# Performance work log

Hardware: AMD Instinct MI355X
Metric: run time of the kernel (lower is better)

## Reference

```python
import jax, jax.numpy as jnp
import numpy as np

B_CAPS, C_CAPS, P_VEC, L_VEC, WIN, ITERS = 1024, 16, 16, 64, 4, 2
BATCH = 4
LOG_2PI = float(np.log(2.0 * np.pi))


def setup_inputs() -> dict:
    key = jax.random.key(0)
    k1, k2, k3, k4 = jax.random.split(key, 4)
    # x packs pose (16*B channels) and activation (B channels)
    x = jax.random.normal(k1, (BATCH, (P_VEC + 1) * B_CAPS, WIN, WIN), dtype=jnp.float32)
    W = 0.01 * jax.random.normal(k2, (C_CAPS, B_CAPS, L_VEC, P_VEC), dtype=jnp.float32)
    beta_v = jax.random.normal(k3, (1,), dtype=jnp.float32)
    beta_a = jax.random.normal(k4, (C_CAPS,), dtype=jnp.float32)
    return {"x": x, "W": W, "beta_v": beta_v, "beta_a": beta_a, "lambda_": jnp.float32(1.0)}


def reference(x, W, beta_v, beta_a, lambda_):
    b = x.shape[0]
    B, C, P, L, K = B_CAPS, C_CAPS, P_VEC, L_VEC, WIN
    N = B * K * K  # total input capsules (every spatial position of every prim capsule)
    # pose: (b, B, K, K, P); activation: (b, N)
    pose = x[:, : P * B].reshape(b, P, B, K, K).transpose(0, 2, 3, 4, 1)
    act = x[:, P * B :].reshape(b, N)
    # votes[b,i,x,y,c,l] = sum_p W[c,i,l,p] * pose[b,i,x,y,p]
    votes = jnp.einsum("cilp,bixyp->bixycl", W, pose)
    V = votes.reshape(b, N, C, L)
    a = act[:, :, None]  # (b, N, 1)
    R = jnp.full((b, N, C), 1.0 / C, dtype=x.dtype)
    mu = a_c = None
    for _ in range(ITERS):
        # ---- M-step: weighted mean / variance over input capsules ----
        r_hat = jnp.clip(R * a, 0.01)                 # (b,N,C)
        sum_r = r_hat.sum(axis=1)                     # (b,C)
        mu = jnp.einsum("bnc,bncl->bcl", r_hat, V) / sum_r[:, :, None]
        sigma = jnp.einsum("bnc,bncl->bcl", r_hat, (V - mu[:, None]) ** 2) / sum_r[:, :, None]
        sigma = jnp.clip(sigma, 0.01)
        cost = (beta_v + jnp.log(sigma)) * sum_r[:, :, None]          # (b,C,L)
        a_c = jax.nn.sigmoid(lambda_ * (beta_a[None, :] - cost.sum(-1)))  # (b,C)
        # ---- E-step (detached in the original: R round-trips through numpy) ----
        # p = prod_l exp(-(V-mu)^2)/sqrt(2*pi*sigma); R = a_c*p / sum_c a_c*p
        # computed in log-space (same math, numerically stable softmax form)
        logp = (-(V - mu[:, None]) ** 2 - 0.5 * (LOG_2PI + jnp.log(sigma[:, None]))).sum(-1)
        R = jax.lax.stop_gradient(jax.nn.softmax(jnp.log(a_c)[:, None, :] + logp, axis=-1))
    mus = mu.reshape(b, C * L, 1, 1)
    acts = a_c.reshape(b, C, 1, 1)
    return jnp.concatenate([mus, acts], axis=1)  # (b, C*L + C, 1, 1)
```

## Files before the change

### kernel.cpp

```cpp
#include <hip/hip_runtime.h>

#define LOG_2PI_F 1.8378770664093453f

constexpr int BC = 1024, CC = 16, PV = 16, LV = 64, BB = 4;
constexpr int CH = (PV + 1) * BC;
constexpr int SLAB = BB * CC * LV;
constexpr int SLABTOT = 2 * SLAB + BB * CC;
constexpr int NB2 = 512;
constexpr int NSLAB_SM = 32;
constexpr size_t WBF_ELEMS = (size_t)CC * BC * LV * PV;
constexpr size_t POSE_ELEMS = (size_t)BC * 64 * 16;
constexpr size_t ACT_ELEMS = (size_t)BC * 64;

typedef __attribute__((ext_vector_type(4))) short short4v;
typedef __attribute__((ext_vector_type(8))) short short8v;
typedef __attribute__((ext_vector_type(16))) float f32x16;

union ABfrag { short8v v; short4v h[2]; unsigned short u[8]; };

__device__ __forceinline__ unsigned short f2bf(float f) {
  unsigned u = __float_as_uint(f);
  u += 0x7fffu + ((u >> 16) & 1u);
  return (unsigned short)(u >> 16);
}

__device__ __forceinline__ short8v cvt8(const float4 a, const float4 b) {
  ABfrag f;
  f.u[0] = f2bf(a.x); f.u[1] = f2bf(a.y); f.u[2] = f2bf(a.z); f.u[3] = f2bf(a.w);
  f.u[4] = f2bf(b.x); f.u[5] = f2bf(b.y); f.u[6] = f2bf(b.z); f.u[7] = f2bf(b.w);
  return f.v;
}

template <int PASS>
__global__ __launch_bounds__(512, 4) void em_sweep2(
    const float* __restrict__ x, const float* __restrict__ W,
    const float* __restrict__ SredIn, const float* __restrict__ beta_v,
    const float* __restrict__ beta_a, const float* __restrict__ lam,
    float* __restrict__ Spart,
    unsigned short* __restrict__ WbfC, unsigned short* __restrict__ poseC,
    float* __restrict__ actC) {
  const int bid = blockIdx.x, t = threadIdx.x;
  const int w = t >> 6, lane = t & 63;
  const int ln31 = lane & 31, h = lane >> 5;
  const int cbase = 2 * w;

  float* slab = Spart + (size_t)bid * SLABTOT;

  __shared__ __align__(16) unsigned short pbf[2][64][20];
  __shared__ float act_s[2][64];
  __shared__ float T_s[64];
  __shared__ float sr_s[64];
  __shared__ float sc_s[64][17];
  __shared__ float rh2[16][64];
  __shared__ __align__(16) float mu_s[64][64];
  __shared__ float lsum_s[64][8];
  __shared__ float Sacc[SLABTOT];

  if (PASS == 1) {
    if (t < 256) {
      const int cap = t >> 7, tt = t & 127;
      const int r = tt >> 1, half = tt & 1;
      const int i = bid + cap * NB2;
      const int4 v = *reinterpret_cast<const int4*>(
          poseC + ((size_t)i * 64 + r) * 16 + 8 * half);
      union { int4 q; short4v s[2]; } u;
      u.q = v;
      *reinterpret_cast<short4v*>(&pbf[cap][r][8 * half]) = u.s[0];
      *reinterpret_cast<short4v*>(&pbf[cap][r][8 * half + 4]) = u.s[1];
    }
    if (t < 128) {
      const int cap = t >> 6, r = t & 63;
      act_s[cap][r] = actC[(size_t)(bid + cap * NB2) * 64 + r];
    }
    if (t < 64) sr_s[t] = 0.f;
    {
      const int bc = t >> 3, part = t & 7;
      const float inv = 1.f / SredIn[2 * SLAB + bc];
      float lsl = 0.f;
#pragma unroll
      for (int q = 0; q < 8; ++q) {
        const int idx = bc * 64 + part * 8 + q;
        const float m = SredIn[idx] * inv;
        const float s2 = fmaxf(SredIn[SLAB + idx] * inv - m * m, 0.01f);
        lsl += logf(s2);
        mu_s[bc][part * 8 + q] = m;
      }
      lsum_s[bc][part] = lsl;
    }
    __syncthreads();
    if (t < 64) {
      float lsum = 0.f;
#pragma unroll
      for (int q = 0; q < 8; ++q) lsum += lsum_s[t][q];
      const float sr = SredIn[2 * SLAB + t];
      const float z = lam[0] * (beta_a[t & 15] - (64.f * beta_v[0] + lsum) * sr);
      const float ac = 1.f / (1.f + expf(-z));
      T_s[t] = logf(ac) - 0.5f * (64.f * LOG_2PI_F + lsum);
    }
    __syncthreads();
  } else {
    {
      const int cap = t >> 8, tt = t & 255;
      const int b = tt >> 6, p = (tt >> 2) & 15, q = tt & 3;
      const int i = bid + cap * NB2;
      const float4 v = *reinterpret_cast<const float4*>(
          x + ((size_t)(b * CH + p * BC + i)) * 16 + 4 * q);
      pbf[cap][b * 16 + 4 * q + 0][p] = f2bf(v.x);
      pbf[cap][b * 16 + 4 * q + 1][p] = f2bf(v.y);
      pbf[cap][b * 16 + 4 * q + 2][p] = f2bf(v.z);
      pbf[cap][b * 16 + 4 * q + 3][p] = f2bf(v.w);
    }
    if (t < 128) {
      const int cap = t >> 6, r = t & 63;
      const int b = r >> 4, xy = r & 15;
      const float a = x[((size_t)(b * CH + PV * BC + bid + cap * NB2)) * 16 + xy];
      act_s[cap][r] = a;
      actC[(size_t)(bid + cap * NB2) * 64 + r] = a;
    }
    __syncthreads();
    if (t < 256) {
      const int cap = t >> 7, tt = t & 127;
      const int r = tt >> 1, half = tt & 1;
      const int i = bid + cap * NB2;
      union { int4 q; short4v s[2]; } u;
      u.s[0] = *reinterpret_cast<const short4v*>(&pbf[cap][r][8 * half]);
      u.s[1] = *reinterpret_cast<const short4v*>(&pbf[cap][r][8 * half + 4]);
      *reinterpret_cast<int4*>(poseC + ((size_t)i * 64 + r) * 16 + 8 * half) = u.q;
    }
  }

  const f32x16 zero16 = {};

#pragma unroll
  for (int cap = 0; cap < 2; ++cap) {
    const int i = bid + cap * NB2;
    short8v wf[4];
    if (PASS == 1) {
#pragma unroll
      for (int k = 0; k < 4; ++k) {
        const int cl_ = k >> 1, lh = k & 1;
        const size_t off = ((size_t)(cbase + cl_) * BC + i) * 1024 +
                           (lh * 32 + ln31) * 16 + 8 * h;
        wf[k] = *reinterpret_cast<const short8v*>(WbfC + off);
      }
    } else {
#pragma unroll
      for (int k = 0; k < 4; ++k) {
        const int cl_ = k >> 1, lh = k & 1;
        const float* src = W + ((size_t)(cbase + cl_) * BC + i) * 1024 +
                           (lh * 32 + ln31) * 16 + 8 * h;
        const float4 v0 = *reinterpret_cast<const float4*>(src);
        const float4 v1 = *reinterpret_cast<const float4*>(src + 4);
        wf[k] = cvt8(v0, v1);
      }
    }
#pragma unroll
    for (int k = 0; k < 4; ++k) asm volatile("" : "+v"(wf[k]));
    if (PASS == 0) {
#pragma unroll
      for (int k = 0; k < 4; ++k) {
        const int cl_ = k >> 1, lh = k & 1;
        const size_t off = ((size_t)(cbase + cl_) * BC + i) * 1024 +
                           (lh * 32 + ln31) * 16 + 8 * h;
        *reinterpret_cast<short8v*>(WbfC + off) = wf[k];
      }
    }

    if (PASS == 1) {
#pragma unroll
      for (int rowhalf = 0; rowhalf < 2; ++rowhalf) {
        ABfrag A;
        {
          const int r = rowhalf * 32 + ln31;
          A.h[0] = *reinterpret_cast<const short4v*>(&pbf[cap][r][8 * h]);
          A.h[1] = *reinterpret_cast<const short4v*>(&pbf[cap][r][8 * h + 4]);
        }
        const int b = (rowhalf * 32 + ln31) >> 4;
#pragma unroll
        for (int cl_ = 0; cl_ < 2; ++cl_) {
          float sc = 0.f;
#pragma unroll
          for (int lh = 0; lh < 2; ++lh) {
            const f32x16 acc = __builtin_amdgcn_mfma_f32_32x32x16_bf16(
                wf[cl_ * 2 + lh], A.v, zero16, 0, 0, 0);
            const float* mrow = &mu_s[b * CC + cbase + cl_][lh * 32 + 4 * h];
#pragma unroll
            for (int g = 0; g < 4; ++g) {
              const float4 m4 = *reinterpret_cast<const float4*>(mrow + 8 * g);
              float d;
              d = acc[4 * g + 0] - m4.x; sc = fmaf(d, d, sc);
              d = acc[4 * g + 1] - m4.y; sc = fmaf(d, d, sc);
              d = acc[4 * g + 2] - m4.z; sc = fmaf(d, d, sc);
              d = acc[4 * g + 3] - m4.w; sc = fmaf(d, d, sc);
            }
          }
          sc += __shfl_xor(sc, 32, 64);
          if (h == 0) sc_s[rowhalf * 32 + ln31][cbase + cl_] = sc;
        }
      }
      __syncthreads();
      {
        const int r = t & 63, cq = t >> 6, b = r >> 4;
        float s[16];
#pragma unroll
        for (int cc = 0; cc < 16; ++cc) s[cc] = T_s[b * CC + cc] - sc_s[r][cc];
        float m = s[0];
#pragma unroll
        for (int cc = 1; cc < 16; ++cc) m = fmaxf(m, s[cc]);
        float den = 0.f;
#pragma unroll
        for (int cc = 0; cc < 16; ++cc) { s[cc] = __expf(s[cc] - m); den += s[cc]; }
        const float a = act_s[cap][r] / den;
#pragma unroll
        for (int k = 0; k < 2; ++k) {
          const int cc = 2 * cq + k;
          const float rh = fmaxf(s[cc] * a, 0.01f);
          rh2[cc][r] = rh;
          atomicAdd(&sr_s[b * CC + cc], rh);
        }
      }
      __syncthreads();
    }

#pragma unroll
    for (int pair = 0; pair < 2; ++pair) {
      ABfrag A;
      {
        const int r = pair * 32 + ln31;
        A.h[0] = *reinterpret_cast<const short4v*>(&pbf[cap][r][8 * h]);
        A.h[1] = *reinterpret_cast<const short4v*>(&pbf[cap][r][8 * h + 4]);
      }
      float p1[4][2] = {}, p2[4][2] = {};
#pragma unroll
      for (int cl_ = 0; cl_ < 2; ++cl_) {
        float rq[16];
        if (PASS == 1) {
#pragma unroll
          for (int g = 0; g < 4; ++g) {
            const float4 v = *reinterpret_cast<const float4*>(
                &rh2[cbase + cl_][pair * 32 + 8 * g + 4 * h]);
            rq[4 * g + 0] = v.x; rq[4 * g + 1] = v.y;
            rq[4 * g + 2] = v.z; rq[4 * g + 3] = v.w;
          }
        } else {
#pragma unroll
          for (int g = 0; g < 4; ++g) {
            const float4 v = *reinterpret_cast<const float4*>(
                &act_s[cap][pair * 32 + 8 * g + 4 * h]);
            rq[4 * g + 0] = fmaxf(v.x * 0.0625f, 0.01f);
            rq[4 * g + 1] = fmaxf(v.y * 0.0625f, 0.01f);
            rq[4 * g + 2] = fmaxf(v.z * 0.0625f, 0.01f);
            rq[4 * g + 3] = fmaxf(v.w * 0.0625f, 0.01f);
          }
        }
#pragma unroll
        for (int lh = 0; lh < 2; ++lh) {
          const f32x16 acc = __builtin_amdgcn_mfma_f32_32x32x16_bf16(
              A.v, wf[cl_ * 2 + lh], zero16, 0, 0, 0);
          const int t4 = cl_ * 2 + lh;
#pragma unroll
          for (int j = 0; j < 16; ++j) {
            const float v = acc[j];
            const float rv = rq[j] * v;
            p1[t4][j >> 3] += rv;
            p2[t4][j >> 3] = fmaf(rv, v, p2[t4][j >> 3]);
          }
        }
      }
#pragma unroll
      for (int t4 = 0; t4 < 4; ++t4)
#pragma unroll
        for (int bh = 0; bh < 2; ++bh) {
          float v1 = p1[t4][bh]; v1 += __shfl_xor(v1, 32, 64);
          float v2 = p2[t4][bh]; v2 += __shfl_xor(v2, 32, 64);
          const int b = pair * 2 + bh, c = cbase + (t4 >> 1);
          const int idx = (b * CC + c) * LV + (t4 & 1) * 32 + ln31;
          if (h == 0) {
            if (cap == 0) { Sacc[idx] = v1; Sacc[SLAB + idx] = v2; }
            else          { Sacc[idx] += v1; Sacc[SLAB + idx] += v2; }
          }
        }
    }
  }

  if (PASS == 1) {
    if (t < 64) Sacc[2 * SLAB + t] = sr_s[t];
  } else {
    if (t < 64) {
      const int b = t >> 4;
      float s = 0.f;
#pragma unroll
      for (int cp = 0; cp < 2; ++cp)
#pragma unroll
        for (int xy = 0; xy < 16; ++xy)
          s += fmaxf(act_s[cp][b * 16 + xy] * 0.0625f, 0.01f);
      Sacc[2 * SLAB + t] = s;
    }
  }
  __syncthreads();
  for (int idx = t; idx < SLABTOT; idx += 512) slab[idx] = Sacc[idx];
}

__global__ void reduce_stageA(const float* __restrict__ Spart,
                              float* __restrict__ Spart2) {
  const int idx = blockIdx.x * 256 + threadIdx.x;
  if (idx >= SLABTOT) return;
  const float* base = Spart + (size_t)(blockIdx.y * 32) * SLABTOT + idx;
  float a = 0.f;
#pragma unroll 8
  for (int s = 0; s < 32; ++s) a += base[(size_t)s * SLABTOT];
  Spart2[(size_t)blockIdx.y * SLABTOT + idx] = a;
}

__global__ void reduce_stageB(const float* __restrict__ Spart2,
                              float* __restrict__ Sred, int nchunk) {
  const int idx = blockIdx.x * 256 + threadIdx.x;
  if (idx >= SLABTOT) return;
  float a = 0.f;
  for (int s = 0; s < nchunk; ++s) a += Spart2[(size_t)s * SLABTOT + idx];
  Sred[idx] = a;
}

__global__ void stats_final(const float* __restrict__ Sred,
                            const float* __restrict__ beta_v,
                            const float* __restrict__ beta_a,
                            const float* __restrict__ lam,
                            float* __restrict__ out) {
  __shared__ float lsum_s[64][8];
  const int t = threadIdx.x;
  const int bc = t >> 3, part = t & 7;
  const float inv = 1.f / Sred[2 * SLAB + bc];
  float lsl = 0.f;
#pragma unroll
  for (int q = 0; q < 8; ++q) {
    const int l = part * 8 + q;
    const int idx = bc * 64 + l;
    const float m = Sred[idx] * inv;
    const float s2 = fmaxf(Sred[SLAB + idx] * inv - m * m, 0.01f);
    lsl += logf(s2);
    out[(size_t)(bc >> 4) * 1040 + (bc & 15) * 64 + l] = m;
  }
  lsum_s[bc][part] = lsl;
  __syncthreads();
  if (t < 64) {
    float lsum = 0.f;
#pragma unroll
    for (int q = 0; q < 8; ++q) lsum += lsum_s[t][q];
    const float sr = Sred[2 * SLAB + t];
    const float z = lam[0] * (beta_a[t & 15] - (64.f * beta_v[0] + lsum) * sr);
    out[(size_t)(t >> 4) * 1040 + 1024 + (t & 15)] = 1.f / (1.f + expf(-z));
  }
}

template <int PASS>
__global__ __launch_bounds__(512, 4) void em_sweep_legacy(
    const float* __restrict__ x, const float* __restrict__ W,
    const float* __restrict__ mu, const float* __restrict__ T,
    float* __restrict__ Spart, int nslab) {
  const int i = blockIdx.x, t = threadIdx.x;
  const int w = t >> 6, lane = t & 63;
  const int ln31 = lane & 31, h = lane >> 5;
  const int cbase = 2 * w;

  float* S1p = Spart + (size_t)(i % nslab) * SLABTOT;
  float* S2p = S1p + SLAB;
  float* Srp = S1p + 2 * SLAB;

  __shared__ __align__(16) unsigned short pbf[64][20];
  __shared__ float act_s[64];
  __shared__ float T_s[64];
  __shared__ float sr_s[64];
  __shared__ float sc_s[64][17];
  __shared__ float rh2[16][64];
  __shared__ __align__(16) float mu_s[64][64];

  short8v wf[4];
#pragma unroll
  for (int k = 0; k < 4; ++k) {
    const int cl_ = k >> 1, lh = k & 1;
    const float* src = W + ((size_t)(cbase + cl_) * BC + i) * 1024 +
                       (lh * 32 + ln31) * 16 + 8 * h;
    const float4 v0 = *reinterpret_cast<const float4*>(src);
    const float4 v1 = *reinterpret_cast<const float4*>(src + 4);
    wf[k] = cvt8(v0, v1);
  }
#pragma unroll
  for (int k = 0; k < 4; ++k) asm volatile("" : "+v"(wf[k]));

  if (t < 256) {
    const int b = t >> 6, p = (t >> 2) & 15, q = t & 3;
    const float4 v = *reinterpret_cast<const float4*>(
        x + ((size_t)(b * CH + p * BC + i)) * 16 + 4 * q);
    pbf[b * 16 + 4 * q + 0][p] = f2bf(v.x);
    pbf[b * 16 + 4 * q + 1][p] = f2bf(v.y);
    pbf[b * 16 + 4 * q + 2][p] = f2bf(v.z);
    pbf[b * 16 + 4 * q + 3][p] = f2bf(v.w);
  }
  if (t < 64) {
    const int b = t >> 4, xy = t & 15;
    act_s[t] = x[((size_t)(b * CH + PV * BC + i)) * 16 + xy];
    if (PASS == 1) { T_s[t] = T[t]; sr_s[t] = 0.f; }
  }
  if (PASS == 1) {
    const float4* msrc = reinterpret_cast<const float4*>(mu);
    float4* mdst = reinterpret_cast<float4*>(&mu_s[0][0]);
    mdst[t] = msrc[t];
    mdst[t + 512] = msrc[t + 512];
  }
  __syncthreads();

  const f32x16 zero16 = {};

  if (PASS == 1) {
#pragma unroll
    for (int rowhalf = 0; rowhalf < 2; ++rowhalf) {
      ABfrag A;
      {
        const int r = rowhalf * 32 + ln31;
        A.h[0] = *reinterpret_cast<const short4v*>(&pbf[r][8 * h]);
        A.h[1] = *reinterpret_cast<const short4v*>(&pbf[r][8 * h + 4]);
      }
      const int b = (rowhalf * 32 + ln31) >> 4;
#pragma unroll
      for (int cl_ = 0; cl_ < 2; ++cl_) {
        float sc = 0.f;
#pragma unroll
        for (int lh = 0; lh < 2; ++lh) {
          const f32x16 acc = __builtin_amdgcn_mfma_f32_32x32x16_bf16(
              wf[cl_ * 2 + lh], A.v, zero16, 0, 0, 0);
          const float* mrow = &mu_s[b * CC + cbase + cl_][lh * 32 + 4 * h];
#pragma unroll
          for (int g = 0; g < 4; ++g) {
            const float4 m4 = *reinterpret_cast<const float4*>(mrow + 8 * g);
            float d;
            d = acc[4 * g + 0] - m4.x; sc = fmaf(d, d, sc);
            d = acc[4 * g + 1] - m4.y; sc = fmaf(d, d, sc);
            d = acc[4 * g + 2] - m4.z; sc = fmaf(d, d, sc);
            d = acc[4 * g + 3] - m4.w; sc = fmaf(d, d, sc);
          }
        }
        sc += __shfl_xor(sc, 32, 64);
        if (h == 0) sc_s[rowhalf * 32 + ln31][cbase + cl_] = sc;
      }
    }
    __syncthreads();
    {
      const int r = t & 63, cq = t >> 6, b = r >> 4;
      float s[16];
#pragma unroll
      for (int cc = 0; cc < 16; ++cc) s[cc] = T_s[b * CC + cc] - sc_s[r][cc];
      float m = s[0];
#pragma unroll
      for (int cc = 1; cc < 16; ++cc) m = fmaxf(m, s[cc]);
      float den = 0.f;
#pragma unroll
      for (int cc = 0; cc < 16; ++cc) { s[cc] = __expf(s[cc] - m); den += s[cc]; }
      const float a = act_s[r] / den;
#pragma unroll
      for (int k = 0; k < 2; ++k) {
        const int cc = 2 * cq + k;
        const float rh = fmaxf(s[cc] * a, 0.01f);
        rh2[cc][r] = rh;
        atomicAdd(&sr_s[b * CC + cc], rh);
      }
    }
    __syncthreads();
  }

#pragma unroll
  for (int pair = 0; pair < 2; ++pair) {
    ABfrag A;
    {
      const int r = pair * 32 + ln31;
      A.h[0] = *reinterpret_cast<const short4v*>(&pbf[r][8 * h]);
      A.h[1] = *reinterpret_cast<const short4v*>(&pbf[r][8 * h + 4]);
    }
    float p1[4][2] = {}, p2[4][2] = {};
#pragma unroll
    for (int cl_ = 0; cl_ < 2; ++cl_) {
      float rq[16];
      if (PASS == 1) {
#pragma unroll
        for (int g = 0; g < 4; ++g) {
          const float4 v = *reinterpret_cast<const float4*>(
              &rh2[cbase + cl_][pair * 32 + 8 * g + 4 * h]);
          rq[4 * g + 0] = v.x; rq[4 * g + 1] = v.y;
          rq[4 * g + 2] = v.z; rq[4 * g + 3] = v.w;
        }
      } else {
#pragma unroll
        for (int g = 0; g < 4; ++g) {
          const float4 v = *reinterpret_cast<const float4*>(
              &act_s[pair * 32 + 8 * g + 4 * h]);
          rq[4 * g + 0] = fmaxf(v.x * 0.0625f, 0.01f);
          rq[4 * g + 1] = fmaxf(v.y * 0.0625f, 0.01f);
          rq[4 * g + 2] = fmaxf(v.z * 0.0625f, 0.01f);
          rq[4 * g + 3] = fmaxf(v.w * 0.0625f, 0.01f);
        }
      }
#pragma unroll
      for (int lh = 0; lh < 2; ++lh) {
        const f32x16 acc = __builtin_amdgcn_mfma_f32_32x32x16_bf16(
            A.v, wf[cl_ * 2 + lh], zero16, 0, 0, 0);
        const int t4 = cl_ * 2 + lh;
#pragma unroll
        for (int j = 0; j < 16; ++j) {
          const float v = acc[j];
          const float rv = rq[j] * v;
          p1[t4][j >> 3] += rv;
          p2[t4][j >> 3] = fmaf(rv, v, p2[t4][j >> 3]);
        }
      }
    }
#pragma unroll
    for (int t4 = 0; t4 < 4; ++t4)
#pragma unroll
      for (int bh = 0; bh < 2; ++bh) {
        float v1 = p1[t4][bh]; v1 += __shfl_xor(v1, 32, 64);
        float v2 = p2[t4][bh]; v2 += __shfl_xor(v2, 32, 64);
        const int b = pair * 2 + bh, c = cbase + (t4 >> 1);
        const int idx = (b * CC + c) * LV + (t4 & 1) * 32 + ln31;
        if (h == 0) { atomicAdd(&S1p[idx], v1); atomicAdd(&S2p[idx], v2); }
      }
  }

  if (PASS == 1) {
    if (t < 64) atomicAdd(&Srp[t], sr_s[t]);
  } else {
    if (t < 64) {
      const int b = t >> 4;
      float s = 0.f;
#pragma unroll
      for (int xy = 0; xy < 16; ++xy) s += fmaxf(act_s[b * 16 + xy] * 0.0625f, 0.01f);
      atomicAdd(&Srp[t], s);
    }
  }
}

__global__ void reduce_slabs(const float* __restrict__ Spart, float* __restrict__ Sred,
                             int nslab, int chunk) {
  const int idx = blockIdx.x * 256 + threadIdx.x;
  if (idx >= SLABTOT) return;
  const int s0 = blockIdx.y * chunk;
  const int s1 = min(s0 + chunk, nslab);
  float a = 0.f;
#pragma unroll 8
  for (int s = s0; s < s1; s++) a += Spart[(size_t)s * SLABTOT + idx];
  atomicAdd(&Sred[idx], a);
}

template <int FINAL>
__global__ void stats_post(const float* __restrict__ Sred,
                           const float* __restrict__ beta_v,
                           const float* __restrict__ beta_a,
                           const float* __restrict__ lam,
                           float* __restrict__ mu_out, float* __restrict__ T_out,
                           float* __restrict__ out) {
  __shared__ float lsum_s[64][8];
  const int t = threadIdx.x;
  const int bc = t >> 3, part = t & 7;
  const float inv = 1.f / Sred[2 * SLAB + bc];
  float lsl = 0.f;
#pragma unroll
  for (int q = 0; q < 8; ++q) {
    const int l = part * 8 + q;
    const int idx = bc * 64 + l;
    const float m = Sred[idx] * inv;
    const float s2 = fmaxf(Sred[SLAB + idx] * inv - m * m, 0.01f);
    lsl += logf(s2);
    if (FINAL) out[(size_t)(bc >> 4) * 1040 + (bc & 15) * 64 + l] = m;
    else mu_out[idx] = m;
  }
  lsum_s[bc][part] = lsl;
  __syncthreads();
  if (t < 64) {
    float lsum = 0.f;
#pragma unroll
    for (int q = 0; q < 8; ++q) lsum += lsum_s[t][q];
    const float sr = Sred[2 * SLAB + t];
    const float z = lam[0] * (beta_a[t & 15] - (64.f * beta_v[0] + lsum) * sr);
    const float ac = 1.f / (1.f + expf(-z));
    if (FINAL) out[(size_t)(t >> 4) * 1040 + 1024 + (t & 15)] = ac;
    else T_out[t] = logf(ac) - 0.5f * (64.f * LOG_2PI_F + lsum);
  }
}

extern "C" void kernel_launch(void* const* d_in, const int* in_sizes, int n_in,
                              void* d_out, int out_size, void* d_ws, size_t ws_size,
                              hipStream_t stream) {
  const float* x = (const float*)d_in[0];
  const float* W = (const float*)d_in[1];
  const float* beta_v = (const float*)d_in[2];
  const float* beta_a = (const float*)d_in[3];
  const float* lam = (const float*)d_in[4];
  float* out = (float*)d_out;

  const size_t need_cache =
      ((size_t)NB2 * SLABTOT + SLABTOT) * sizeof(float) + WBF_ELEMS * 2 +
      POSE_ELEMS * 2 + ACT_ELEMS * sizeof(float) +
      (size_t)16 * SLABTOT * sizeof(float);

  float* Spart = (float*)d_ws;

  if (ws_size >= need_cache) {
    float* Sred = Spart + (size_t)NB2 * SLABTOT;
    unsigned short* WbfC = (unsigned short*)(Sred + SLABTOT);
    unsigned short* poseC = WbfC + WBF_ELEMS;
    float* actC = (float*)(poseC + POSE_ELEMS);
    float* Spart2 = actC + ACT_ELEMS;

    const dim3 agrid((SLABTOT + 255) / 256, 16);
    const dim3 bgrid((SLABTOT + 255) / 256);
    em_sweep2<0><<<dim3(NB2), dim3(512), 0, stream>>>(
        x, W, nullptr, beta_v, beta_a, lam, Spart, WbfC, poseC, actC);
    reduce_stageA<<<agrid, dim3(256), 0, stream>>>(Spart, Spart2);
    reduce_stageB<<<bgrid, dim3(256), 0, stream>>>(Spart2, Sred, 16);
    em_sweep2<1><<<dim3(NB2), dim3(512), 0, stream>>>(
        x, W, Sred, beta_v, beta_a, lam, Spart, WbfC, poseC, actC);
    reduce_stageA<<<agrid, dim3(256), 0, stream>>>(Spart, Spart2);
    reduce_stageB<<<bgrid, dim3(256), 0, stream>>>(Spart2, Sred, 16);
    stats_final<<<dim3(1), dim3(512), 0, stream>>>(Sred, beta_v, beta_a, lam, out);
    return;
  }

  const int nslab = NSLAB_SM;
  float* Sred = Spart + (size_t)nslab * SLABTOT;
  float* muW = Sred + SLABTOT;
  float* Tw = muW + SLAB;
  const int chunk = 32;
  const dim3 rgrid((SLABTOT + 255) / 256, (nslab + chunk - 1) / chunk);

  hipMemsetAsync(Spart, 0, (size_t)nslab * SLABTOT * sizeof(float), stream);
  hipMemsetAsync(Sred, 0, SLABTOT * sizeof(float), stream);
  em_sweep_legacy<0><<<dim3(BC), dim3(512), 0, stream>>>(x, W, nullptr, nullptr, Spart, nslab);
  reduce_slabs<<<rgrid, dim3(256), 0, stream>>>(Spart, Sred, nslab, chunk);
  stats_post<0><<<dim3(1), dim3(512), 0, stream>>>(Sred, beta_v, beta_a, lam, muW, Tw, nullptr);

  hipMemsetAsync(Spart, 0, (size_t)nslab * SLABTOT * sizeof(float), stream);
  em_sweep_legacy<1><<<dim3(BC), dim3(512), 0, stream>>>(x, W, muW, Tw, Spart, nslab);
  hipMemsetAsync(Sred, 0, SLABTOT * sizeof(float), stream);
  reduce_slabs<<<rgrid, dim3(256), 0, stream>>>(Spart, Sred, nslab, chunk);
  stats_post<1><<<dim3(1), dim3(512), 0, stream>>>(Sred, beta_v, beta_a, lam, nullptr, nullptr, out);
}
```

Baseline: 80.66 us.

## Use 1024-thread blocks with one output capsule per wave in EM sweep

The block size of both EM sweep launches doubles from 512 to 1024 threads, so each of 16 waves handles one output capsule instead of two. Per-wave work and register footprint for weight fragments and accumulators are halved, which is meant to expose more parallelism and latency hiding. The cost is more waves contending for the same LDS, more synchronisation per block, and possibly lower blocks per CU given the shared memory footprint. Setup phases that assume 512 threads are guarded with t<512.

```diff
diff --git a/kernel.cpp b/kernel.cpp
--- a/kernel.cpp
+++ b/kernel.cpp
@@ -32,7 +32,7 @@
 }
 
 template <int PASS>
-__global__ __launch_bounds__(512, 4) void em_sweep2(
+__global__ __launch_bounds__(1024, 4) void em_sweep2(
     const float* __restrict__ x, const float* __restrict__ W,
     const float* __restrict__ SredIn, const float* __restrict__ beta_v,
     const float* __restrict__ beta_a, const float* __restrict__ lam,
@@ -40,9 +40,10 @@
     unsigned short* __restrict__ WbfC, unsigned short* __restrict__ poseC,
     float* __restrict__ actC) {
   const int bid = blockIdx.x, t = threadIdx.x;
-  const int w = t >> 6, lane = t & 63;
+  const int w = t >> 6;
+  const int lane = t & 63;
   const int ln31 = lane & 31, h = lane >> 5;
-  const int cbase = 2 * w;
+  const int c = w;
 
   float* slab = Spart + (size_t)bid * SLABTOT;
 
@@ -73,7 +74,7 @@
       act_s[cap][r] = actC[(size_t)(bid + cap * NB2) * 64 + r];
     }
     if (t < 64) sr_s[t] = 0.f;
-    {
+    if (t < 512) {
       const int bc = t >> 3, part = t & 7;
       const float inv = 1.f / SredIn[2 * SLAB + bc];
       float lsl = 0.f;
@@ -99,7 +100,7 @@
     }
     __syncthreads();
   } else {
-    {
+    if (t < 512) {
       const int cap = t >> 8, tt = t & 255;
       const int b = tt >> 6, p = (tt >> 2) & 15, q = tt & 3;
       const int i = bid + cap * NB2;
@@ -134,34 +135,31 @@
 #pragma unroll
   for (int cap = 0; cap < 2; ++cap) {
     const int i = bid + cap * NB2;
-    short8v wf[4];
+    short8v wf[2];
     if (PASS == 1) {
 #pragma unroll
-      for (int k = 0; k < 4; ++k) {
-        const int cl_ = k >> 1, lh = k & 1;
-        const size_t off = ((size_t)(cbase + cl_) * BC + i) * 1024 +
-                           (lh * 32 + ln31) * 16 + 8 * h;
+      for (int k = 0; k < 2; ++k) {
+        const size_t off = ((size_t)c * BC + i) * 1024 +
+                           (k * 32 + ln31) * 16 + 8 * h;
         wf[k] = *reinterpret_cast<const short8v*>(WbfC + off);
       }
     } else {
 #pragma unroll
-      for (int k = 0; k < 4; ++k) {
-        const int cl_ = k >> 1, lh = k & 1;
-        const float* src = W + ((size_t)(cbase + cl_) * BC + i) * 1024 +
-                           (lh * 32 + ln31) * 16 + 8 * h;
+      for (int k = 0; k < 2; ++k) {
+        const float* src = W + ((size_t)c * BC + i) * 1024 +
+                           (k * 32 + ln31) * 16 + 8 * h;
         const float4 v0 = *reinterpret_cast<const float4*>(src);
         const float4 v1 = *reinterpret_cast<const float4*>(src + 4);
         wf[k] = cvt8(v0, v1);
       }
     }
 #pragma unroll
-    for (int k = 0; k < 4; ++k) asm volatile("" : "+v"(wf[k]));
+    for (int k = 0; k < 2; ++k) asm volatile("" : "+v"(wf[k]));
     if (PASS == 0) {
 #pragma unroll
-      for (int k = 0; k < 4; ++k) {
-        const int cl_ = k >> 1, lh = k & 1;
-        const size_t off = ((size_t)(cbase + cl_) * BC + i) * 1024 +
-                           (lh * 32 + ln31) * 16 + 8 * h;
+      for (int k = 0; k < 2; ++k) {
+        const size_t off = ((size_t)c * BC + i) * 1024 +
+                           (k * 32 + ln31) * 16 + 8 * h;
         *reinterpret_cast<short8v*>(WbfC + off) = wf[k];
       }
     }
@@ -176,27 +174,24 @@
           A.h[1] = *reinterpret_cast<const short4v*>(&pbf[cap][r][8 * h + 4]);
         }
         const int b = (rowhalf * 32 + ln31) >> 4;
-#pragma unroll
-        for (int cl_ = 0; cl_ < 2; ++cl_) {
-          float sc = 0.f;
-#pragma unroll
-          for (int lh = 0; lh < 2; ++lh) {
-            const f32x16 acc = __builtin_amdgcn_mfma_f32_32x32x16_bf16(
-                wf[cl_ * 2 + lh], A.v, zero16, 0, 0, 0);
-            const float* mrow = &mu_s[b * CC + cbase + cl_][lh * 32 + 4 * h];
-#pragma unroll
-            for (int g = 0; g < 4; ++g) {
-              const float4 m4 = *reinterpret_cast<const float4*>(mrow + 8 * g);
-              float d;
-              d = acc[4 * g + 0] - m4.x; sc = fmaf(d, d, sc);
-              d = acc[4 * g + 1] - m4.y; sc = fmaf(d, d, sc);
-              d = acc[4 * g + 2] - m4.z; sc = fmaf(d, d, sc);
-              d = acc[4 * g + 3] - m4.w; sc = fmaf(d, d, sc);
-            }
+        float sc = 0.f;
+#pragma unroll
+        for (int lh = 0; lh < 2; ++lh) {
+          const f32x16 acc = __builtin_amdgcn_mfma_f32_32x32x16_bf16(
+              wf[lh], A.v, zero16, 0, 0, 0);
+          const float* mrow = &mu_s[b * CC + c][lh * 32 + 4 * h];
+#pragma unroll
+          for (int g = 0; g < 4; ++g) {
+            const float4 m4 = *reinterpret_cast<const float4*>(mrow + 8 * g);
+            float d;
+            d = acc[4 * g + 0] - m4.x; sc = fmaf(d, d, sc);
+            d = acc[4 * g + 1] - m4.y; sc = fmaf(d, d, sc);
+            d = acc[4 * g + 2] - m4.z; sc = fmaf(d, d, sc);
+            d = acc[4 * g + 3] - m4.w; sc = fmaf(d, d, sc);
           }
-          sc += __shfl_xor(sc, 32, 64);
-          if (h == 0) sc_s[rowhalf * 32 + ln31][cbase + cl_] = sc;
-        }
+        }
+        sc += __shfl_xor(sc, 32, 64);
+        if (h == 0) sc_s[rowhalf * 32 + ln31][c] = sc;
       }
       __syncthreads();
       {
@@ -211,13 +206,9 @@
 #pragma unroll
         for (int cc = 0; cc < 16; ++cc) { s[cc] = __expf(s[cc] - m); den += s[cc]; }
         const float a = act_s[cap][r] / den;
-#pragma unroll
-        for (int k = 0; k < 2; ++k) {
-          const int cc = 2 * cq + k;
-          const float rh = fmaxf(s[cc] * a, 0.01f);
-          rh2[cc][r] = rh;
-          atomicAdd(&sr_s[b * CC + cc], rh);
-        }
+        const float rh = fmaxf(s[cq] * a, 0.01f);
+        rh2[cq][r] = rh;
+        atomicAdd(&sr_s[b * CC + cq], rh);
       }
       __syncthreads();
     }
@@ -230,51 +221,47 @@
         A.h[0] = *reinterpret_cast<const short4v*>(&pbf[cap][r][8 * h]);
         A.h[1] = *reinterpret_cast<const short4v*>(&pbf[cap][r][8 * h + 4]);
       }
-      float p1[4][2] = {}, p2[4][2] = {};
-#pragma unroll
-      for (int cl_ = 0; cl_ < 2; ++cl_) {
-        float rq[16];
-        if (PASS == 1) {
-#pragma unroll
-          for (int g = 0; g < 4; ++g) {
-            const float4 v = *reinterpret_cast<const float4*>(
-                &rh2[cbase + cl_][pair * 32 + 8 * g + 4 * h]);
-            rq[4 * g + 0] = v.x; rq[4 * g + 1] = v.y;
-            rq[4 * g + 2] = v.z; rq[4 * g + 3] = v.w;
-          }
-        } else {
-#pragma unroll
-          for (int g = 0; g < 4; ++g) {
-            const float4 v = *reinterpret_cast<const float4*>(
-                &act_s[cap][pair * 32 + 8 * g + 4 * h]);
-            rq[4 * g + 0] = fmaxf(v.x * 0.0625f, 0.01f);
-            rq[4 * g + 1] = fmaxf(v.y * 0.0625f, 0.01f);
-            rq[4 * g + 2] = fmaxf(v.z * 0.0625f, 0.01f);
-            rq[4 * g + 3] = fmaxf(v.w * 0.0625f, 0.01f);
-          }
-        }
-#pragma unroll
-        for (int lh = 0; lh < 2; ++lh) {
-          const f32x16 acc = __builtin_amdgcn_mfma_f32_32x32x16_bf16(
-              A.v, wf[cl_ * 2 + lh], zero16, 0, 0, 0);
-          const int t4 = cl_ * 2 + lh;
-#pragma unroll
-          for (int j = 0; j < 16; ++j) {
-            const float v = acc[j];
-            const float rv = rq[j] * v;
-            p1[t4][j >> 3] += rv;
-            p2[t4][j >> 3] = fmaf(rv, v, p2[t4][j >> 3]);
-          }
-        }
-      }
-#pragma unroll
-      for (int t4 = 0; t4 < 4; ++t4)
+      float rq[16];
+      if (PASS == 1) {
+#pragma unroll
+        for (int g = 0; g < 4; ++g) {
+          const float4 v = *reinterpret_cast<const float4*>(
+              &rh2[c][pair * 32 + 8 * g + 4 * h]);
+          rq[4 * g + 0] = v.x; rq[4 * g + 1] = v.y;
+          rq[4 * g + 2] = v.z; rq[4 * g + 3] = v.w;
+        }
+      } else {
+#pragma unroll
+        for (int g = 0; g < 4; ++g) {
+          const float4 v = *reinterpret_cast<const float4*>(
+              &act_s[cap][pair * 32 + 8 * g + 4 * h]);
+          rq[4 * g + 0] = fmaxf(v.x * 0.0625f, 0.01f);
+          rq[4 * g + 1] = fmaxf(v.y * 0.0625f, 0.01f);
+          rq[4 * g + 2] = fmaxf(v.z * 0.0625f, 0.01f);
+          rq[4 * g + 3] = fmaxf(v.w * 0.0625f, 0.01f);
+        }
+      }
+      float p1[2][2] = {}, p2[2][2] = {};
+#pragma unroll
+      for (int lh = 0; lh < 2; ++lh) {
+        const f32x16 acc = __builtin_amdgcn_mfma_f32_32x32x16_bf16(
+            A.v, wf[lh], zero16, 0, 0, 0);
+#pragma unroll
+        for (int j = 0; j < 16; ++j) {
+          const float v = acc[j];
+          const float rv = rq[j] * v;
+          p1[lh][j >> 3] += rv;
+          p2[lh][j >> 3] = fmaf(rv, v, p2[lh][j >> 3]);
+        }
+      }
+#pragma unroll
+      for (int lh = 0; lh < 2; ++lh)
 #pragma unroll
         for (int bh = 0; bh < 2; ++bh) {
-          float v1 = p1[t4][bh]; v1 += __shfl_xor(v1, 32, 64);
-          float v2 = p2[t4][bh]; v2 += __shfl_xor(v2, 32, 64);
-          const int b = pair * 2 + bh, c = cbase + (t4 >> 1);
-          const int idx = (b * CC + c) * LV + (t4 & 1) * 32 + ln31;
+          float v1 = p1[lh][bh]; v1 += __shfl_xor(v1, 32, 64);
+          float v2 = p2[lh][bh]; v2 += __shfl_xor(v2, 32, 64);
+          const int b = pair * 2 + bh;
+          const int idx = (b * CC + c) * LV + lh * 32 + ln31;
           if (h == 0) {
             if (cap == 0) { Sacc[idx] = v1; Sacc[SLAB + idx] = v2; }
             else          { Sacc[idx] += v1; Sacc[SLAB + idx] += v2; }
@@ -298,7 +285,7 @@
     }
   }
   __syncthreads();
-  for (int idx = t; idx < SLABTOT; idx += 512) slab[idx] = Sacc[idx];
+  for (int idx = t; idx < SLABTOT; idx += 1024) slab[idx] = Sacc[idx];
 }
 
 __global__ void reduce_stageA(const float* __restrict__ Spart,
@@ -611,11 +598,11 @@
 
     const dim3 agrid((SLABTOT + 255) / 256, 16);
     const dim3 bgrid((SLABTOT + 255) / 256);
-    em_sweep2<0><<<dim3(NB2), dim3(512), 0, stream>>>(
+    em_sweep2<0><<<dim3(NB2), dim3(1024), 0, stream>>>(
         x, W, nullptr, beta_v, beta_a, lam, Spart, WbfC, poseC, actC);
     reduce_stageA<<<agrid, dim3(256), 0, stream>>>(Spart, Spart2);
     reduce_stageB<<<bgrid, dim3(256), 0, stream>>>(Spart2, Sred, 16);
-    em_sweep2<1><<<dim3(NB2), dim3(512), 0, stream>>>(
+    em_sweep2<1><<<dim3(NB2), dim3(1024), 0, stream>>>(
         x, W, Sred, beta_v, beta_a, lam, Spart, WbfC, poseC, actC);
     reduce_stageA<<<agrid, dim3(256), 0, stream>>>(Spart, Spart2);
     reduce_stageB<<<bgrid, dim3(256), 0, stream>>>(Spart2, Sred, 16);
```

Result: slower. 83.34 us (+3.3%).

## Batch both capsules per phase in PASS 1 to halve block barriers

Applied to the files above, without the earlier changes.

The PASS 1 path is split out and restructured so the squared-distance phase, the softmax/responsibility phase and the weighted-moment phase each handle both capsules at once. The sc_s and rh2 shared buffers are doubled per capsule, which cuts the per-capsule __syncthreads pairs to one barrier per phase. In exchange it uses more LDS (about 8 KB extra), which may lower occupancy, and it reloads the W fragments from global memory in the third phase.

```diff
diff --git a/kernel.cpp b/kernel.cpp
--- a/kernel.cpp
+++ b/kernel.cpp
@@ -50,11 +50,13 @@
   __shared__ float act_s[2][64];
   __shared__ float T_s[64];
   __shared__ float sr_s[64];
-  __shared__ float sc_s[64][17];
-  __shared__ float rh2[16][64];
+  __shared__ float sc_s[2][64][17];
+  __shared__ __align__(16) float rh2[2][16][64];
   __shared__ __align__(16) float mu_s[64][64];
   __shared__ float lsum_s[64][8];
   __shared__ float Sacc[SLABTOT];
+
+  const f32x16 zero16 = {};
 
   if (PASS == 1) {
     if (t < 256) {
@@ -98,6 +100,135 @@
       T_s[t] = logf(ac) - 0.5f * (64.f * LOG_2PI_F + lsum);
     }
     __syncthreads();
+
+#pragma unroll
+    for (int cap = 0; cap < 2; ++cap) {
+      const int i = bid + cap * NB2;
+      short8v wf[4];
+#pragma unroll
+      for (int k = 0; k < 4; ++k) {
+        const int cl_ = k >> 1, lh = k & 1;
+        const size_t off = ((size_t)(cbase + cl_) * BC + i) * 1024 +
+                           (lh * 32 + ln31) * 16 + 8 * h;
+        wf[k] = *reinterpret_cast<const short8v*>(WbfC + off);
+      }
+#pragma unroll
+      for (int rowhalf = 0; rowhalf < 2; ++rowhalf) {
+        ABfrag A;
+        {
+          const int r = rowhalf * 32 + ln31;
+          A.h[0] = *reinterpret_cast<const short4v*>(&pbf[cap][r][8 * h]);
+          A.h[1] = *reinterpret_cast<const short4v*>(&pbf[cap][r][8 * h + 4]);
+        }
+        const int b = (rowhalf * 32 + ln31) >> 4;
+#pragma unroll
+        for (int cl_ = 0; cl_ < 2; ++cl_) {
+          float sc = 0.f;
+#pragma unroll
+          for (int lh = 0; lh < 2; ++lh) {
+            const f32x16 acc = __builtin_amdgcn_mfma_f32_32x32x16_bf16(
+                wf[cl_ * 2 + lh], A.v, zero16, 0, 0, 0);
+            const float* mrow = &mu_s[b * CC + cbase + cl_][lh * 32 + 4 * h];
+#pragma unroll
+            for (int g = 0; g < 4; ++g) {
+              const float4 m4 = *reinterpret_cast<const float4*>(mrow + 8 * g);
+              float d;
+              d = acc[4 * g + 0] - m4.x; sc = fmaf(d, d, sc);
+              d = acc[4 * g + 1] - m4.y; sc = fmaf(d, d, sc);
+              d = acc[4 * g + 2] - m4.z; sc = fmaf(d, d, sc);
+              d = acc[4 * g + 3] - m4.w; sc = fmaf(d, d, sc);
+            }
+          }
+          sc += __shfl_xor(sc, 32, 64);
+          if (h == 0) sc_s[cap][rowhalf * 32 + ln31][cbase + cl_] = sc;
+        }
+      }
+    }
+    __syncthreads();
+
+#pragma unroll
+    for (int cap = 0; cap < 2; ++cap) {
+      const int r = t & 63, cq = t >> 6, b = r >> 4;
+      float s[16];
+#pragma unroll
+      for (int cc = 0; cc < 16; ++cc) s[cc] = T_s[b * CC + cc] - sc_s[cap][r][cc];
+      float m = s[0];
+#pragma unroll
+      for (int cc = 1; cc < 16; ++cc) m = fmaxf(m, s[cc]);
+      float den = 0.f;
+#pragma unroll
+      for (int cc = 0; cc < 16; ++cc) { s[cc] = __expf(s[cc] - m); den += s[cc]; }
+      const float a = act_s[cap][r] / den;
+#pragma unroll
+      for (int k = 0; k < 2; ++k) {
+        const int cc = 2 * cq + k;
+        const float rh = fmaxf(s[cc] * a, 0.01f);
+        rh2[cap][cc][r] = rh;
+        atomicAdd(&sr_s[b * CC + cc], rh);
+      }
+    }
+    __syncthreads();
+
+#pragma unroll
+    for (int cap = 0; cap < 2; ++cap) {
+      const int i = bid + cap * NB2;
+      short8v wf[4];
+#pragma unroll
+      for (int k = 0; k < 4; ++k) {
+        const int cl_ = k >> 1, lh = k & 1;
+        const size_t off = ((size_t)(cbase + cl_) * BC + i) * 1024 +
+                           (lh * 32 + ln31) * 16 + 8 * h;
+        wf[k] = *reinterpret_cast<const short8v*>(WbfC + off);
+      }
+#pragma unroll
+      for (int pair = 0; pair < 2; ++pair) {
+        ABfrag A;
+        {
+          const int r = pair * 32 + ln31;
+          A.h[0] = *reinterpret_cast<const short4v*>(&pbf[cap][r][8 * h]);
+          A.h[1] = *reinterpret_cast<const short4v*>(&pbf[cap][r][8 * h + 4]);
+        }
+        float p1[4][2] = {}, p2[4][2] = {};
+#pragma unroll
+        for (int cl_ = 0; cl_ < 2; ++cl_) {
+          float rq[16];
+#pragma unroll
+          for (int g = 0; g < 4; ++g) {
+            const float4 v = *reinterpret_cast<const float4*>(
+                &rh2[cap][cbase + cl_][pair * 32 + 8 * g + 4 * h]);
+            rq[4 * g + 0] = v.x; rq[4 * g + 1] = v.y;
+            rq[4 * g + 2] = v.z; rq[4 * g + 3] = v.w;
+          }
+#pragma unroll
+          for (int lh = 0; lh < 2; ++lh) {
+            const f32x16 acc = __builtin_amdgcn_mfma_f32_32x32x16_bf16(
+                A.v, wf[cl_ * 2 + lh], zero16, 0, 0, 0);
+            const int t4 = cl_ * 2 + lh;
+#pragma unroll
+            for (int j = 0; j < 16; ++j) {
+              const float v = acc[j];
+              const float rv = rq[j] * v;
+              p1[t4][j >> 3] += rv;
+              p2[t4][j >> 3] = fmaf(rv, v, p2[t4][j >> 3]);
+            }
+          }
+        }
+#pragma unroll
+        for (int t4 = 0; t4 < 4; ++t4)
+#pragma unroll
+          for (int bh = 0; bh < 2; ++bh) {
+            float v1 = p1[t4][bh]; v1 += __shfl_xor(v1, 32, 64);
+            float v2 = p2[t4][bh]; v2 += __shfl_xor(v2, 32, 64);
+            const int b = pair * 2 + bh, c = cbase + (t4 >> 1);
+            const int idx = (b * CC + c) * LV + (t4 & 1) * 32 + ln31;
+            if (h == 0) {
+              if (cap == 0) { Sacc[idx] = v1; Sacc[SLAB + idx] = v2; }
+              else          { Sacc[idx] += v1; Sacc[SLAB + idx] += v2; }
+            }
+          }
+      }
+    }
+    if (t < 64) Sacc[2 * SLAB + t] = sr_s[t];
   } else {
     {
       const int cap = t >> 8, tt = t & 255;
@@ -127,23 +258,11 @@
       u.s[1] = *reinterpret_cast<const short4v*>(&pbf[cap][r][8 * half + 4]);
       *reinterpret_cast<int4*>(poseC + ((size_t)i * 64 + r) * 16 + 8 * half) = u.q;
     }
-  }
-
-  const f32x16 zero16 = {};
-
-#pragma unroll
-  for (int cap = 0; cap < 2; ++cap) {
-    const int i = bid + cap * NB2;
-    short8v wf[4];
-    if (PASS == 1) {
-#pragma unroll
-      for (int k = 0; k < 4; ++k) {
-        const int cl_ = k >> 1, lh = k & 1;
-        const size_t off = ((size_t)(cbase + cl_) * BC + i) * 1024 +
-                           (lh * 32 + ln31) * 16 + 8 * h;
-        wf[k] = *reinterpret_cast<const short8v*>(WbfC + off);
-      }
-    } else {
+
+#pragma unroll
+    for (int cap = 0; cap < 2; ++cap) {
+      const int i = bid + cap * NB2;
+      short8v wf[4];
 #pragma unroll
       for (int k = 0; k < 4; ++k) {
         const int cl_ = k >> 1, lh = k & 1;
@@ -153,10 +272,8 @@
         const float4 v1 = *reinterpret_cast<const float4*>(src + 4);
         wf[k] = cvt8(v0, v1);
       }
-    }
-#pragma unroll
-    for (int k = 0; k < 4; ++k) asm volatile("" : "+v"(wf[k]));
-    if (PASS == 0) {
+#pragma unroll
+      for (int k = 0; k < 4; ++k) asm volatile("" : "+v"(wf[k]));
 #pragma unroll
       for (int k = 0; k < 4; ++k) {
         const int cl_ = k >> 1, lh = k & 1;
@@ -164,85 +281,19 @@
                            (lh * 32 + ln31) * 16 + 8 * h;
         *reinterpret_cast<short8v*>(WbfC + off) = wf[k];
       }
-    }
-
-    if (PASS == 1) {
-#pragma unroll
-      for (int rowhalf = 0; rowhalf < 2; ++rowhalf) {
+
+#pragma unroll
+      for (int pair = 0; pair < 2; ++pair) {
         ABfrag A;
         {
-          const int r = rowhalf * 32 + ln31;
+          const int r = pair * 32 + ln31;
           A.h[0] = *reinterpret_cast<const short4v*>(&pbf[cap][r][8 * h]);
           A.h[1] = *reinterpret_cast<const short4v*>(&pbf[cap][r][8 * h + 4]);
         }
-        const int b = (rowhalf * 32 + ln31) >> 4;
+        float p1[4][2] = {}, p2[4][2] = {};
 #pragma unroll
         for (int cl_ = 0; cl_ < 2; ++cl_) {
-          float sc = 0.f;
-#pragma unroll
-          for (int lh = 0; lh < 2; ++lh) {
-            const f32x16 acc = __builtin_amdgcn_mfma_f32_32x32x16_bf16(
-                wf[cl_ * 2 + lh], A.v, zero16, 0, 0, 0);
-            const float* mrow = &mu_s[b * CC + cbase + cl_][lh * 32 + 4 * h];
-#pragma unroll
-            for (int g = 0; g < 4; ++g) {
-              const float4 m4 = *reinterpret_cast<const float4*>(mrow + 8 * g);
-              float d;
-              d = acc[4 * g + 0] - m4.x; sc = fmaf(d, d, sc);
-              d = acc[4 * g + 1] - m4.y; sc = fmaf(d, d, sc);
-              d = acc[4 * g + 2] - m4.z; sc = fmaf(d, d, sc);
-              d = acc[4 * g + 3] - m4.w; sc = fmaf(d, d, sc);
-            }
-          }
-          sc += __shfl_xor(sc, 32, 64);
-          if (h == 0) sc_s[rowhalf * 32 + ln31][cbase + cl_] = sc;
-        }
-      }
-      __syncthreads();
-      {
-        const int r = t & 63, cq = t >> 6, b = r >> 4;
-        float s[16];
-#pragma unroll
-        for (int cc = 0; cc < 16; ++cc) s[cc] = T_s[b * CC + cc] - sc_s[r][cc];
-        float m = s[0];
-#pragma unroll
-        for (int cc = 1; cc < 16; ++cc) m = fmaxf(m, s[cc]);
-        float den = 0.f;
-#pragma unroll
-        for (int cc = 0; cc < 16; ++cc) { s[cc] = __expf(s[cc] - m); den += s[cc]; }
-        const float a = act_s[cap][r] / den;
-#pragma unroll
-        for (int k = 0; k < 2; ++k) {
-          const int cc = 2 * cq + k;
-          const float rh = fmaxf(s[cc] * a, 0.01f);
-          rh2[cc][r] = rh;
-          atomicAdd(&sr_s[b * CC + cc], rh);
-        }
-      }
-      __syncthreads();
-    }
-
-#pragma unroll
-    for (int pair = 0; pair < 2; ++pair) {
-      ABfrag A;
-      {
-        const int r = pair * 32 + ln31;
-        A.h[0] = *reinterpret_cast<const short4v*>(&pbf[cap][r][8 * h]);
-        A.h[1] = *reinterpret_cast<const short4v*>(&pbf[cap][r][8 * h + 4]);
-      }
-      float p1[4][2] = {}, p2[4][2] = {};
-#pragma unroll
-      for (int cl_ = 0; cl_ < 2; ++cl_) {
-        float rq[16];
-        if (PASS == 1) {
-#pragma unroll
-          for (int g = 0; g < 4; ++g) {
-            const float4 v = *reinterpret_cast<const float4*>(
-                &rh2[cbase + cl_][pair * 32 + 8 * g + 4 * h]);
-            rq[4 * g + 0] = v.x; rq[4 * g + 1] = v.y;
-            rq[4 * g + 2] = v.z; rq[4 * g + 3] = v.w;
-          }
-        } else {
+          float rq[16];
 #pragma unroll
           for (int g = 0; g < 4; ++g) {
             const float4 v = *reinterpret_cast<const float4*>(
@@ -252,40 +303,35 @@
             rq[4 * g + 2] = fmaxf(v.z * 0.0625f, 0.01f);
             rq[4 * g + 3] = fmaxf(v.w * 0.0625f, 0.01f);
           }
-        }
-#pragma unroll
-        for (int lh = 0; lh < 2; ++lh) {
-          const f32x16 acc = __builtin_amdgcn_mfma_f32_32x32x16_bf16(
-              A.v, wf[cl_ * 2 + lh], zero16, 0, 0, 0);
-          const int t4 = cl_ * 2 + lh;
-#pragma unroll
-          for (int j = 0; j < 16; ++j) {
-            const float v = acc[j];
-            const float rv = rq[j] * v;
-            p1[t4][j >> 3] += rv;
-            p2[t4][j >> 3] = fmaf(rv, v, p2[t4][j >> 3]);
-          }
-        }
-      }
-#pragma unroll
-      for (int t4 = 0; t4 < 4; ++t4)
-#pragma unroll
-        for (int bh = 0; bh < 2; ++bh) {
-          float v1 = p1[t4][bh]; v1 += __shfl_xor(v1, 32, 64);
-          float v2 = p2[t4][bh]; v2 += __shfl_xor(v2, 32, 64);
-          const int b = pair * 2 + bh, c = cbase + (t4 >> 1);
-          const int idx = (b * CC + c) * LV + (t4 & 1) * 32 + ln31;
-          if (h == 0) {
-            if (cap == 0) { Sacc[idx] = v1; Sacc[SLAB + idx] = v2; }
-            else          { Sacc[idx] += v1; Sacc[SLAB + idx] += v2; }
-          }
-        }
-    }
-  }
-
-  if (PASS == 1) {
-    if (t < 64) Sacc[2 * SLAB + t] = sr_s[t];
-  } else {
+#pragma unroll
+          for (int lh = 0; lh < 2; ++lh) {
+            const f32x16 acc = __builtin_amdgcn_mfma_f32_32x32x16_bf16(
+                A.v, wf[cl_ * 2 + lh], zero16, 0, 0, 0);
+            const int t4 = cl_ * 2 + lh;
+#pragma unroll
+            for (int j = 0; j < 16; ++j) {
+              const float v = acc[j];
+              const float rv = rq[j] * v;
+              p1[t4][j >> 3] += rv;
+              p2[t4][j >> 3] = fmaf(rv, v, p2[t4][j >> 3]);
+            }
+          }
+        }
+#pragma unroll
+        for (int t4 = 0; t4 < 4; ++t4)
+#pragma unroll
+          for (int bh = 0; bh < 2; ++bh) {
+            float v1 = p1[t4][bh]; v1 += __shfl_xor(v1, 32, 64);
+            float v2 = p2[t4][bh]; v2 += __shfl_xor(v2, 32, 64);
+            const int b = pair * 2 + bh, c = cbase + (t4 >> 1);
+            const int idx = (b * CC + c) * LV + (t4 & 1) * 32 + ln31;
+            if (h == 0) {
+              if (cap == 0) { Sacc[idx] = v1; Sacc[SLAB + idx] = v2; }
+              else          { Sacc[idx] += v1; Sacc[SLAB + idx] += v2; }
+            }
+          }
+      }
+    }
     if (t < 64) {
       const int b = t >> 4;
       float s = 0.f;
@@ -297,6 +343,7 @@
       Sacc[2 * SLAB + t] = s;
     }
   }
+
   __syncthreads();
   for (int idx = t; idx < SLABTOT; idx += 512) slab[idx] = Sacc[idx];
 }
```

Result: faster. 78.86 us (-2.2%).
